# Optimization experiments

Measured on AMD Instinct MI355X. Metric: run time of the kernel, lower is better.

Reference implementation:

```python
import jax, jax.numpy as jnp
import numpy as np

CONF_THRESHOLD = 0.1
CONF_PERCENTILE = 0.5  # 50.0 / 100
VOXEL_SCALES = (10.0, 20.0, 40.0)
ADAPTIVE_LAMBDA = 20.0  # median of voxel_scales
K = 1024                # coords per axis for packing (coords are < ~lambda * extent_ratio << 1024)
SENTINEL = K * K * K    # key for invalid points; > any packed key, fits int32


def setup_inputs() -> dict:
    key = jax.random.key(0)
    k1, k2 = jax.random.split(key)
    world_points = jax.random.normal(k1, (1, 64, 384, 384, 3), dtype=jnp.float32)
    world_points_conf = jax.random.uniform(k2, (1, 64, 384, 384), dtype=jnp.float32)
    return {"world_points": world_points, "world_points_conf": world_points_conf}


def _unique_voxel_counts(pts, valid, pmin, min_extent, voxel_lambda):
    # pts: [S, N, 3], valid: [S, N]
    voxel_size = min_extent / voxel_lambda
    coords = jnp.floor((pts - pmin) / voxel_size).astype(jnp.int32)
    coords = jnp.clip(coords, 0, K - 1)
    packed = (coords[..., 0] * K + coords[..., 1]) * K + coords[..., 2]  # [S, N]
    keys = jnp.where(valid, packed, SENTINEL)
    skeys = jnp.sort(keys, axis=1)
    prev = jnp.concatenate([jnp.full((skeys.shape[0], 1), -1, skeys.dtype), skeys[:, :-1]], axis=1)
    is_new = (skeys != prev) & (skeys < SENTINEL)
    return jnp.sum(is_new, axis=1).astype(jnp.int32)  # [S] unique voxels per frame


def reference(world_points, world_points_conf):
    wp = world_points[0]            # [S, H, W, 3]
    conf = world_points_conf[0]     # [S, H, W]
    S = wp.shape[0]
    pts = wp.reshape(S, -1, 3)      # [S, N, 3]
    c = conf.reshape(S, -1)         # [S, N]

    # per-frame confidence gating: conf > threshold AND conf >= per-frame median
    q = jnp.quantile(c, CONF_PERCENTILE, axis=1, keepdims=True)
    valid = (c > CONF_THRESHOLD) & (c >= q)  # [S, N]

    # global bbox over all valid points (across frames)
    BIG = jnp.float32(1e30)
    vmask = valid[..., None]
    pmin = jnp.min(jnp.where(vmask, pts, BIG), axis=(0, 1))    # [3]
    pmax = jnp.max(jnp.where(vmask, pts, -BIG), axis=(0, 1))   # [3]
    min_extent = jnp.min(pmax - pmin)

    scales = list(VOXEL_SCALES) + [ADAPTIVE_LAMBDA]
    counts = jnp.stack([
        _unique_voxel_counts(pts, valid, pmin, min_extent, lam) for lam in scales
    ], axis=0)  # [n_scales + 1(adaptive), S]

    # scene complexity: std(depths of conf>thr points, unbiased) * density
    mask = (c > CONF_THRESHOLD).astype(pts.dtype)
    depths = jnp.linalg.norm(pts, axis=-1)  # [S, N]
    n = jnp.sum(mask)
    mean_d = jnp.sum(depths * mask) / n
    var_d = jnp.sum(mask * (depths - mean_d) ** 2) / (n - 1.0)  # Bessel, matches torch .std()
    complexity = jnp.sqrt(var_d) * jnp.mean(mask)

    return counts, complexity
```

## Files before the change

kernel.cpp:

```cpp
#include <hip/hip_runtime.h>
#include <cstdint>

#define S_FRAMES 64
#define NPF      147456
#define TOT      (S_FRAMES * NPF)
#define NBINS    4096
#define R1       73728u
#define NB1      512
#define CHK      (NPF / 8)
#define G4       (CHK / 4)
#define CAPC     512
#define CAPR     4096
#define LCAPR    1024
#define LCAPC    128
#define WORDS_BM 9344

#define OFF_HSL  0
#define OFF_CSL  (OFF_HSL + NB1 * NBINS * 4)
#define OFF_PBD  (OFF_CSL + NB1 * 384 * 4)
#define OFF_PBC  (OFF_PBD + NB1 * 16)
#define OFF_CTR  (OFF_PBC + NB1 * 4)
#define OFF_HDR  (OFF_CTR + 128 * 4)
#define OFF_CAND (OFF_HDR + 128 * 4)
#define OFF_RECI (OFF_CAND + S_FRAMES * CAPC * 4)
#define OFF_RECV (OFF_RECI + S_FRAMES * CAPR * 4)
#define OFF_MED  (OFF_RECV + S_FRAMES * CAPR * 4)
#define OFF_FBB  (OFF_MED + 256)
#define OFF_VSL  (((OFF_FBB + S_FRAMES * 6 * 4) + 15) & ~15)

__device__ __forceinline__ int conf_bin(float v) {
    int b = (int)(v * (float)NBINS);
    return b < 0 ? 0 : (b > NBINS - 1 ? NBINS - 1 : b);
}
__device__ __forceinline__ uint32_t encf(float f) {
    uint32_t u = __float_as_uint(f);
    return (u & 0x80000000u) ? ~u : (u | 0x80000000u);
}
__device__ __forceinline__ float decf(uint32_t e) {
    uint32_t u = (e & 0x80000000u) ? (e & 0x7FFFFFFFu) : ~e;
    return __uint_as_float(u);
}

__global__ __launch_bounds__(256) void k_pass1(const float* __restrict__ conf,
                                               const float* __restrict__ pts,
                                               uint32_t* __restrict__ hsl,
                                               uint32_t* __restrict__ csl,
                                               double* __restrict__ pbd,
                                               uint32_t* __restrict__ pbc,
                                               uint32_t* __restrict__ ctr) {
    int f = blockIdx.x >> 3, chunk = blockIdx.x & 7;
    __shared__ uint32_t h[NBINS];
    __shared__ uint32_t cmn[192], cmx[192];
    for (int i = threadIdx.x; i < NBINS; i += 256) h[i] = 0;
    for (int i = threadIdx.x; i < 192; i += 256) { cmn[i] = 0xFFFFFFFFu; cmx[i] = 0u; }
    if (chunk == 0 && threadIdx.x < 2) ctr[f + threadIdx.x * 64] = 0u;
    __syncthreads();

    const size_t base = (size_t)f * NPF + (size_t)chunk * CHK;
    const float4* c4 = (const float4*)(conf + base);
    const float4* p4 = (const float4*)(pts + base * 3);
    double s1 = 0.0, s2 = 0.0;
    uint32_t cnt = 0;
    for (int i = threadIdx.x; i < G4; i += 256) {
        float4 cc = c4[i];
        float4 a = p4[3 * (size_t)i], b = p4[3 * (size_t)i + 1], d = p4[3 * (size_t)i + 2];
        float cv[4] = {cc.x, cc.y, cc.z, cc.w};
        float v[12] = {a.x, a.y, a.z, a.w, b.x, b.y, b.z, b.w, d.x, d.y, d.z, d.w};
        #pragma unroll
        for (int j = 0; j < 4; j++) {
            float c = cv[j];
            int fb = conf_bin(c);
            atomicAdd(&h[fb], 1u);
            if (c > 0.1f) {
                float x = v[3 * j], y = v[3 * j + 1], z = v[3 * j + 2];
                float dd = sqrtf(x * x + y * y + z * z);
                s1 += (double)dd;
                s2 += (double)dd * (double)dd;
                cnt++;
                int cb3 = (fb >> 6) * 3;
                atomicMin(&cmn[cb3 + 0], encf(x));
                atomicMin(&cmn[cb3 + 1], encf(y));
                atomicMin(&cmn[cb3 + 2], encf(z));
                atomicMax(&cmx[cb3 + 0], encf(x));
                atomicMax(&cmx[cb3 + 1], encf(y));
                atomicMax(&cmx[cb3 + 2], encf(z));
            }
        }
    }
    __syncthreads();
    uint32_t* gh = hsl + (size_t)blockIdx.x * NBINS;
    for (int i = threadIdx.x; i < NBINS; i += 256) gh[i] = h[i];
    uint32_t* gc = csl + (size_t)blockIdx.x * 384;
    for (int i = threadIdx.x; i < 192; i += 256) { gc[i] = cmn[i]; gc[192 + i] = cmx[i]; }

    for (int o = 32; o > 0; o >>= 1) {
        s1 += __shfl_xor(s1, o); s2 += __shfl_xor(s2, o); cnt += __shfl_xor(cnt, o);
    }
    __shared__ double rd[2][4];
    __shared__ uint32_t rc[4];
    int wave = threadIdx.x >> 6, lane = threadIdx.x & 63;
    if (lane == 0) { rd[0][wave] = s1; rd[1][wave] = s2; rc[wave] = cnt; }
    __syncthreads();
    if (threadIdx.x == 0) {
        pbd[2 * (size_t)blockIdx.x]     = rd[0][0] + rd[0][1] + rd[0][2] + rd[0][3];
        pbd[2 * (size_t)blockIdx.x + 1] = rd[1][0] + rd[1][1] + rd[1][2] + rd[1][3];
        pbc[blockIdx.x] = rc[0] + rc[1] + rc[2] + rc[3];
    }
}

__global__ __launch_bounds__(1024) void k_resolve(const float* __restrict__ conf,
                                                  const uint32_t* __restrict__ hsl,
                                                  uint32_t* __restrict__ ctr,
                                                  uint32_t* __restrict__ hdr,
                                                  float* __restrict__ cand,
                                                  uint32_t* __restrict__ reci,
                                                  float* __restrict__ recv) {
    int f = blockIdx.x >> 3, chunk = blockIdx.x & 7;
    const int tid = threadIdx.x;
    __shared__ uint32_t h[NBINS];
    __shared__ uint32_t wsum[16], wexcl[16];
    __shared__ uint32_t binfo[2];
    const uint32_t* hb = hsl + (size_t)(f * 8) * NBINS;
    for (int i = tid; i < NBINS; i += 1024) {
        uint32_t s = 0;
        #pragma unroll
        for (int k = 0; k < 8; k++) s += hb[(size_t)k * NBINS + i];
        h[i] = s;
    }
    __syncthreads();
    const int base = tid * 4;
    uint32_t s = h[base] + h[base + 1] + h[base + 2] + h[base + 3];
    const uint32_t lane = tid & 63, wave = tid >> 6;
    uint32_t scan = s;
    for (int o = 1; o < 64; o <<= 1) {
        uint32_t t = __shfl_up(scan, o);
        if (lane >= o) scan += t;
    }
    if (lane == 63) wsum[wave] = scan;
    __syncthreads();
    if (tid == 0) {
        uint32_t run = 0;
        for (int w = 0; w < 16; w++) { wexcl[w] = run; run += wsum[w]; }
    }
    __syncthreads();
    uint32_t excl = wexcl[wave] + (scan - s);
    if (R1 >= excl && R1 < excl + s) {
        uint32_t cum = excl;
        #pragma unroll
        for (int j = 0; j < 4; j++) {
            uint32_t c2 = h[base + j];
            if (R1 < cum + c2) { binfo[0] = (uint32_t)(base + j); binfo[1] = cum; break; }
            cum += c2;
        }
    }
    __syncthreads();
    const int b1 = (int)binfo[0];
    const int bc = b1 >> 6;
    if (chunk == 0 && tid < 2) hdr[f * 2 + tid] = binfo[tid];

    __shared__ uint32_t l_ri[LCAPR];
    __shared__ float    l_rv[LCAPR];
    __shared__ float    l_cv[LCAPC];
    __shared__ uint32_t l_nr, l_nc, g_base_r, g_base_c;
    if (tid == 0) { l_nr = 0u; l_nc = 0u; }
    __syncthreads();

    uint32_t* ccnt = &ctr[f];
    uint32_t* rcnt = &ctr[64 + f];
    const float4* c4 = (const float4*)(conf + (size_t)f * NPF + (size_t)chunk * CHK);
    for (int i = tid; i < G4; i += 1024) {
        float4 v = c4[i];
        float vv[4] = {v.x, v.y, v.z, v.w};
        #pragma unroll
        for (int j = 0; j < 4; j++) {
            int fb = conf_bin(vv[j]);
            if (fb == b1) {
                uint32_t k = atomicAdd(&l_nc, 1u);
                if (k < LCAPC) l_cv[k] = vv[j];
                else {
                    uint32_t g = atomicAdd(ccnt, 1u);
                    if (g < CAPC) cand[(size_t)f * CAPC + g] = vv[j];
                }
            }
            if ((fb >> 6) == bc) {
                uint32_t k = atomicAdd(&l_nr, 1u);
                if (k < LCAPR) {
                    l_ri[k] = (uint32_t)(chunk * CHK + i * 4 + j);
                    l_rv[k] = vv[j];
                } else {
                    uint32_t g = atomicAdd(rcnt, 1u);
                    if (g < CAPR) {
                        reci[(size_t)f * CAPR + g] = (uint32_t)(chunk * CHK + i * 4 + j);
                        recv[(size_t)f * CAPR + g] = vv[j];
                    }
                }
            }
        }
    }
    __syncthreads();
    if (tid == 0) {
        g_base_c = atomicAdd(ccnt, min(l_nc, (uint32_t)LCAPC));
        g_base_r = atomicAdd(rcnt, min(l_nr, (uint32_t)LCAPR));
    }
    __syncthreads();
    uint32_t nc = min(l_nc, (uint32_t)LCAPC), bcg = g_base_c;
    for (uint32_t i = tid; i < nc; i += 1024) {
        uint32_t g = bcg + i;
        if (g < CAPC) cand[(size_t)f * CAPC + g] = l_cv[i];
    }
    uint32_t nr = min(l_nr, (uint32_t)LCAPR), brg = g_base_r;
    for (uint32_t i = tid; i < nr; i += 1024) {
        uint32_t g = brg + i;
        if (g < CAPR) {
            reci[(size_t)f * CAPR + g] = l_ri[i];
            recv[(size_t)f * CAPR + g] = l_rv[i];
        }
    }
}

__global__ __launch_bounds__(1024) void k_frame(const float* __restrict__ pts,
                                                const uint32_t* __restrict__ hdr,
                                                const uint32_t* __restrict__ ctr,
                                                const float* __restrict__ cand,
                                                const uint32_t* __restrict__ reci,
                                                const float* __restrict__ recv,
                                                const uint32_t* __restrict__ csl,
                                                float* __restrict__ med,
                                                float* __restrict__ fbb) {
    int f = blockIdx.x;
    const int tid = threadIdx.x;
    __shared__ float cbuf[CAPC];
    __shared__ float smed;
    int b1 = (int)hdr[f * 2];
    uint32_t cb1 = hdr[f * 2 + 1];
    int bc = b1 >> 6;
    int m = (int)min(ctr[f], (uint32_t)CAPC);
    for (int i = tid; i < m; i += 1024) cbuf[i] = cand[(size_t)f * CAPC + i];
    __syncthreads();
    int target = (int)(R1 - cb1);
    for (int i = tid; i < m; i += 1024) {
        float v = cbuf[i];
        int r = 0;
        for (int j = 0; j < m; j++) {
            float w = cbuf[j];
            r += (w < v) || (w == v && j < i);
        }
        if (r == target) { smed = v; med[f] = v; }
    }
    __syncthreads();
    float mv = smed;

    float mnx = 1e30f, mny = 1e30f, mnz = 1e30f;
    float mxx = -1e30f, mxy = -1e30f, mxz = -1e30f;
    int rn = (int)min(ctr[64 + f], (uint32_t)CAPR);
    for (int k = tid; k < rn; k += 1024) {
        float v = recv[(size_t)f * CAPR + k];
        if (v > 0.1f && v >= mv) {
            size_t idx = ((size_t)f * NPF + reci[(size_t)f * CAPR + k]) * 3;
            float x = pts[idx], y = pts[idx + 1], z = pts[idx + 2];
            mnx = fminf(mnx, x); mny = fminf(mny, y); mnz = fminf(mnz, z);
            mxx = fmaxf(mxx, x); mxy = fmaxf(mxy, y); mxz = fmaxf(mxz, z);
        }
    }
    if (tid < 64 && tid > bc) {
        uint32_t emn[3] = {0xFFFFFFFFu, 0xFFFFFFFFu, 0xFFFFFFFFu};
        uint32_t emx[3] = {0u, 0u, 0u};
        for (int sI = 0; sI < 8; sI++) {
            const uint32_t* gc = csl + (size_t)(f * 8 + sI) * 384;
            #pragma unroll
            for (int k = 0; k < 3; k++) {
                emn[k] = min(emn[k], gc[tid * 3 + k]);
                emx[k] = max(emx[k], gc[192 + tid * 3 + k]);
            }
        }
        if (emn[0] != 0xFFFFFFFFu) {
            mnx = fminf(mnx, decf(emn[0])); mny = fminf(mny, decf(emn[1]));
            mnz = fminf(mnz, decf(emn[2]));
            mxx = fmaxf(mxx, decf(emx[0])); mxy = fmaxf(mxy, decf(emx[1]));
            mxz = fmaxf(mxz, decf(emx[2]));
        }
    }
    for (int o = 32; o > 0; o >>= 1) {
        mnx = fminf(mnx, __shfl_xor(mnx, o)); mny = fminf(mny, __shfl_xor(mny, o));
        mnz = fminf(mnz, __shfl_xor(mnz, o));
        mxx = fmaxf(mxx, __shfl_xor(mxx, o)); mxy = fmaxf(mxy, __shfl_xor(mxy, o));
        mxz = fmaxf(mxz, __shfl_xor(mxz, o));
    }
    __shared__ float rf[6][16];
    int wave = tid >> 6, lane = tid & 63;
    if (lane == 0) {
        rf[0][wave] = mnx; rf[1][wave] = mny; rf[2][wave] = mnz;
        rf[3][wave] = mxx; rf[4][wave] = mxy; rf[5][wave] = mxz;
    }
    __syncthreads();
    if (tid == 0) {
        float o0 = rf[0][0], o1 = rf[1][0], o2 = rf[2][0];
        float o3 = rf[3][0], o4 = rf[4][0], o5 = rf[5][0];
        for (int w = 1; w < 16; w++) {
            o0 = fminf(o0, rf[0][w]); o1 = fminf(o1, rf[1][w]); o2 = fminf(o2, rf[2][w]);
            o3 = fmaxf(o3, rf[3][w]); o4 = fmaxf(o4, rf[4][w]); o5 = fmaxf(o5, rf[5][w]);
        }
        fbb[f * 6 + 0] = o0; fbb[f * 6 + 1] = o1; fbb[f * 6 + 2] = o2;
        fbb[f * 6 + 3] = o3; fbb[f * 6 + 4] = o4; fbb[f * 6 + 5] = o5;
    }
}

__global__ __launch_bounds__(256) void k_voxel(const float* __restrict__ pts,
                                               const float* __restrict__ conf,
                                               const float* __restrict__ med,
                                               const float* __restrict__ fbb,
                                               uint32_t* __restrict__ vsl) {
    int f = blockIdx.x >> 3;
    int chunk = blockIdx.x & 7;
    __shared__ __align__(16) uint32_t bm[WORDS_BM];
    for (int i = threadIdx.x; i < WORDS_BM; i += 256) bm[i] = 0;
    float pmnx = 1e30f, pmny = 1e30f, pmnz = 1e30f;
    float pmxx = -1e30f, pmxy = -1e30f, pmxz = -1e30f;
    for (int i = 0; i < S_FRAMES; i++) {
        pmnx = fminf(pmnx, fbb[i * 6 + 0]); pmny = fminf(pmny, fbb[i * 6 + 1]);
        pmnz = fminf(pmnz, fbb[i * 6 + 2]);
        pmxx = fmaxf(pmxx, fbb[i * 6 + 3]); pmxy = fmaxf(pmxy, fbb[i * 6 + 4]);
        pmxz = fmaxf(pmxz, fbb[i * 6 + 5]);
    }
    float ex = pmxx - pmnx, ey = pmxy - pmny, ez = pmxz - pmnz;
    float me = fminf(ex, fminf(ey, ez));
    float i40 = 40.0f / me, i20 = 20.0f / me, i10 = 10.0f / me;
    float q = med[f];
    __syncthreads();
    const size_t base = (size_t)f * NPF + (size_t)chunk * CHK;
    const float4* c4 = (const float4*)(conf + base);
    const float4* p4 = (const float4*)(pts + base * 3);
    for (int i = threadIdx.x; i < G4; i += 256) {
        float4 cc = c4[i];
        float4 a = p4[3 * (size_t)i], b = p4[3 * (size_t)i + 1], d = p4[3 * (size_t)i + 2];
        float cv[4] = {cc.x, cc.y, cc.z, cc.w};
        float v[12] = {a.x, a.y, a.z, a.w, b.x, b.y, b.z, b.w, d.x, d.y, d.z, d.w};
        #pragma unroll
        for (int j = 0; j < 4; j++) {
            float c = cv[j];
            if (c > 0.1f && c >= q) {
                float x = v[3 * j] - pmnx, y = v[3 * j + 1] - pmny, z = v[3 * j + 2] - pmnz;
                int cx, cy, cz, bit;
                cx = (int)floorf(x * i40); cy = (int)floorf(y * i40); cz = (int)floorf(z * i40);
                cx = min(max(cx, 0), 63); cy = min(max(cy, 0), 63); cz = min(max(cz, 0), 63);
                bit = (cx << 12) | (cy << 6) | cz;
                atomicOr(&bm[bit >> 5], 1u << (bit & 31));
                cx = (int)floorf(x * i20); cy = (int)floorf(y * i20); cz = (int)floorf(z * i20);
                cx = min(max(cx, 0), 31); cy = min(max(cy, 0), 31); cz = min(max(cz, 0), 31);
                bit = (cx << 10) | (cy << 5) | cz;
                atomicOr(&bm[8192 + (bit >> 5)], 1u << (bit & 31));
                cx = (int)floorf(x * i10); cy = (int)floorf(y * i10); cz = (int)floorf(z * i10);
                cx = min(max(cx, 0), 15); cy = min(max(cy, 0), 15); cz = min(max(cz, 0), 15);
                bit = (cx << 8) | (cy << 4) | cz;
                atomicOr(&bm[9216 + (bit >> 5)], 1u << (bit & 31));
            }
        }
    }
    __syncthreads();
    uint4* dst = (uint4*)(vsl + (size_t)blockIdx.x * WORDS_BM);
    const uint4* src = (const uint4*)bm;
    for (int i = threadIdx.x; i < WORDS_BM / 4; i += 256) dst[i] = src[i];
}

__global__ __launch_bounds__(256) void k_final(const uint32_t* __restrict__ vsl,
                                               const double* __restrict__ pbd,
                                               const uint32_t* __restrict__ pbc,
                                               float* __restrict__ out) {
    int f = blockIdx.x;
    uint32_t c40 = 0, c20 = 0, c10 = 0;
    const uint32_t* fb = vsl + (size_t)(f * 8) * WORDS_BM;
    for (int i = threadIdx.x; i < WORDS_BM / 4; i += 256) {
        uint4 w = ((const uint4*)fb)[i];
        #pragma unroll
        for (int k = 1; k < 8; k++) {
            uint4 u = ((const uint4*)(fb + (size_t)k * WORDS_BM))[i];
            w.x |= u.x; w.y |= u.y; w.z |= u.z; w.w |= u.w;
        }
        uint32_t pc = __popc(w.x) + __popc(w.y) + __popc(w.z) + __popc(w.w);
        if (i < 2048) c40 += pc;
        else if (i < 2304) c20 += pc;
        else c10 += pc;
    }
    for (int o = 32; o > 0; o >>= 1) {
        c40 += __shfl_xor(c40, o);
        c20 += __shfl_xor(c20, o);
        c10 += __shfl_xor(c10, o);
    }
    __shared__ uint32_t red[3][4];
    int wave = threadIdx.x >> 6, lane = threadIdx.x & 63;
    if (lane == 0) { red[0][wave] = c40; red[1][wave] = c20; red[2][wave] = c10; }
    __syncthreads();
    if (threadIdx.x == 0) {
        uint32_t t40 = red[0][0] + red[0][1] + red[0][2] + red[0][3];
        uint32_t t20 = red[1][0] + red[1][1] + red[1][2] + red[1][3];
        uint32_t t10 = red[2][0] + red[2][1] + red[2][2] + red[2][3];
        out[0 * S_FRAMES + f] = (float)t10;
        out[1 * S_FRAMES + f] = (float)t20;
        out[2 * S_FRAMES + f] = (float)t40;
        out[3 * S_FRAMES + f] = (float)t20;
    }
    if (f == 0) {
        double s1 = 0.0, s2 = 0.0;
        uint32_t cnt = 0;
        for (int b = threadIdx.x; b < NB1; b += 256) {
            s1 += pbd[2 * (size_t)b];
            s2 += pbd[2 * (size_t)b + 1];
            cnt += pbc[b];
        }
        for (int o = 32; o > 0; o >>= 1) {
            s1 += __shfl_xor(s1, o); s2 += __shfl_xor(s2, o); cnt += __shfl_xor(cnt, o);
        }
        __shared__ double rd[2][4];
        __shared__ uint32_t rc2[4];
        if (lane == 0) { rd[0][wave] = s1; rd[1][wave] = s2; rc2[wave] = cnt; }
        __syncthreads();
        if (threadIdx.x == 0) {
            double S1 = rd[0][0] + rd[0][1] + rd[0][2] + rd[0][3];
            double S2 = rd[1][0] + rd[1][1] + rd[1][2] + rd[1][3];
            double n = (double)(rc2[0] + rc2[1] + rc2[2] + rc2[3]);
            double mean = S1 / n;
            double var = (S2 - n * mean * mean) / (n - 1.0);
            out[4 * S_FRAMES] = (float)(sqrt(var) * (n / (double)TOT));
        }
    }
}

extern "C" void kernel_launch(void* const* d_in, const int* in_sizes, int n_in,
                              void* d_out, int out_size, void* d_ws, size_t ws_size,
                              hipStream_t stream) {
    const float* pts  = (const float*)d_in[0];
    const float* conf = (const float*)d_in[1];
    float* out = (float*)d_out;
    char* ws = (char*)d_ws;
    uint32_t* hsl  = (uint32_t*)(ws + OFF_HSL);
    uint32_t* csl  = (uint32_t*)(ws + OFF_CSL);
    double*   pbd  = (double*)(ws + OFF_PBD);
    uint32_t* pbc  = (uint32_t*)(ws + OFF_PBC);
    uint32_t* ctr  = (uint32_t*)(ws + OFF_CTR);
    uint32_t* hdr  = (uint32_t*)(ws + OFF_HDR);
    float*    cand = (float*)(ws + OFF_CAND);
    uint32_t* reci = (uint32_t*)(ws + OFF_RECI);
    float*    recv = (float*)(ws + OFF_RECV);
    float*    med  = (float*)(ws + OFF_MED);
    float*    fbb  = (float*)(ws + OFF_FBB);
    uint32_t* vsl  = (uint32_t*)(ws + OFF_VSL);

    k_pass1  <<<NB1,      256,  0, stream>>>(conf, pts, hsl, csl, pbd, pbc, ctr);
    k_resolve<<<NB1,      1024, 0, stream>>>(conf, hsl, ctr, hdr, cand, reci, recv);
    k_frame  <<<S_FRAMES, 1024, 0, stream>>>(pts, hdr, ctr, cand, reci, recv, csl, med, fbb);
    k_voxel  <<<NB1,      256,  0, stream>>>(pts, conf, med, fbb, vsl);
    k_final  <<<S_FRAMES, 256,  0, stream>>>(vsl, pbd, pbc, out);
}
```

Baseline: 105.9 us.

## Split histogram bin search into own kernel and retune per-frame slice counts

```diff
diff --git a/kernel.cpp b/kernel.cpp
--- a/kernel.cpp
+++ b/kernel.cpp
@@ -6,9 +6,22 @@
 #define TOT      (S_FRAMES * NPF)
 #define NBINS    4096
 #define R1       73728u
-#define NB1      512
-#define CHK      (NPF / 8)
-#define G4       (CHK / 4)
+
+#define NSL      32
+#define NB1      (S_FRAMES * NSL)
+#define CHK1     (NPF / NSL)
+#define G41      (CHK1 / 4)
+
+#define NRS      8
+#define NBR      (S_FRAMES * NRS)
+#define CHKR     (NPF / NRS)
+#define G4R      (CHKR / 4)
+
+#define NVS      16
+#define NBV      (S_FRAMES * NVS)
+#define CHKV     (NPF / NVS)
+#define G4V      (CHKV / 4)
+
 #define CAPC     512
 #define CAPR     4096
 #define LCAPR    1024
@@ -48,7 +61,7 @@
                                                double* __restrict__ pbd,
                                                uint32_t* __restrict__ pbc,
                                                uint32_t* __restrict__ ctr) {
-    int f = blockIdx.x >> 3, chunk = blockIdx.x & 7;
+    int f = blockIdx.x >> 5, chunk = blockIdx.x & 31;
     __shared__ uint32_t h[NBINS];
     __shared__ uint32_t cmn[192], cmx[192];
     for (int i = threadIdx.x; i < NBINS; i += 256) h[i] = 0;
@@ -56,12 +69,12 @@
     if (chunk == 0 && threadIdx.x < 2) ctr[f + threadIdx.x * 64] = 0u;
     __syncthreads();
 
-    const size_t base = (size_t)f * NPF + (size_t)chunk * CHK;
+    const size_t base = (size_t)f * NPF + (size_t)chunk * CHK1;
     const float4* c4 = (const float4*)(conf + base);
     const float4* p4 = (const float4*)(pts + base * 3);
     double s1 = 0.0, s2 = 0.0;
     uint32_t cnt = 0;
-    for (int i = threadIdx.x; i < G4; i += 256) {
+    for (int i = threadIdx.x; i < G41; i += 256) {
         float4 cc = c4[i];
         float4 a = p4[3 * (size_t)i], b = p4[3 * (size_t)i + 1], d = p4[3 * (size_t)i + 2];
         float cv[4] = {cc.x, cc.y, cc.z, cc.w};
@@ -108,55 +121,56 @@
     }
 }
 
+__global__ __launch_bounds__(1024) void k_findbin(const uint32_t* __restrict__ hsl,
+                                                  uint32_t* __restrict__ hdr) {
+    int f = blockIdx.x;
+    const int tid = threadIdx.x;
+    const uint32_t* hb = hsl + (size_t)(f * NSL) * NBINS;
+    uint4 acc = make_uint4(0u, 0u, 0u, 0u);
+    for (int s = 0; s < NSL; s++) {
+        uint4 u = *(const uint4*)(hb + (size_t)s * NBINS + tid * 4);
+        acc.x += u.x; acc.y += u.y; acc.z += u.z; acc.w += u.w;
+    }
+    uint32_t s4 = acc.x + acc.y + acc.z + acc.w;
+    const uint32_t lane = tid & 63, wave = tid >> 6;
+    uint32_t scan = s4;
+    for (int o = 1; o < 64; o <<= 1) {
+        uint32_t t = __shfl_up(scan, o);
+        if (lane >= o) scan += t;
+    }
+    __shared__ uint32_t wsum[16], wexcl[16];
+    __shared__ uint32_t binfo[2];
+    if (lane == 63) wsum[wave] = scan;
+    __syncthreads();
+    if (tid == 0) {
+        uint32_t run = 0;
+        for (int w = 0; w < 16; w++) { wexcl[w] = run; run += wsum[w]; }
+    }
+    __syncthreads();
+    uint32_t excl = wexcl[wave] + (scan - s4);
+    if (R1 >= excl && R1 < excl + s4) {
+        uint32_t cum = excl;
+        uint32_t bv[4] = {acc.x, acc.y, acc.z, acc.w};
+        #pragma unroll
+        for (int j = 0; j < 4; j++) {
+            if (R1 < cum + bv[j]) { binfo[0] = (uint32_t)(tid * 4 + j); binfo[1] = cum; break; }
+            cum += bv[j];
+        }
+    }
+    __syncthreads();
+    if (tid < 2) hdr[f * 2 + tid] = binfo[tid];
+}
+
 __global__ __launch_bounds__(1024) void k_resolve(const float* __restrict__ conf,
-                                                  const uint32_t* __restrict__ hsl,
+                                                  const uint32_t* __restrict__ hdr,
                                                   uint32_t* __restrict__ ctr,
-                                                  uint32_t* __restrict__ hdr,
                                                   float* __restrict__ cand,
                                                   uint32_t* __restrict__ reci,
                                                   float* __restrict__ recv) {
     int f = blockIdx.x >> 3, chunk = blockIdx.x & 7;
     const int tid = threadIdx.x;
-    __shared__ uint32_t h[NBINS];
-    __shared__ uint32_t wsum[16], wexcl[16];
-    __shared__ uint32_t binfo[2];
-    const uint32_t* hb = hsl + (size_t)(f * 8) * NBINS;
-    for (int i = tid; i < NBINS; i += 1024) {
-        uint32_t s = 0;
-        #pragma unroll
-        for (int k = 0; k < 8; k++) s += hb[(size_t)k * NBINS + i];
-        h[i] = s;
-    }
-    __syncthreads();
-    const int base = tid * 4;
-    uint32_t s = h[base] + h[base + 1] + h[base + 2] + h[base + 3];
-    const uint32_t lane = tid & 63, wave = tid >> 6;
-    uint32_t scan = s;
-    for (int o = 1; o < 64; o <<= 1) {
-        uint32_t t = __shfl_up(scan, o);
-        if (lane >= o) scan += t;
-    }
-    if (lane == 63) wsum[wave] = scan;
-    __syncthreads();
-    if (tid == 0) {
-        uint32_t run = 0;
-        for (int w = 0; w < 16; w++) { wexcl[w] = run; run += wsum[w]; }
-    }
-    __syncthreads();
-    uint32_t excl = wexcl[wave] + (scan - s);
-    if (R1 >= excl && R1 < excl + s) {
-        uint32_t cum = excl;
-        #pragma unroll
-        for (int j = 0; j < 4; j++) {
-            uint32_t c2 = h[base + j];
-            if (R1 < cum + c2) { binfo[0] = (uint32_t)(base + j); binfo[1] = cum; break; }
-            cum += c2;
-        }
-    }
-    __syncthreads();
-    const int b1 = (int)binfo[0];
+    const int b1 = (int)hdr[f * 2];
     const int bc = b1 >> 6;
-    if (chunk == 0 && tid < 2) hdr[f * 2 + tid] = binfo[tid];
 
     __shared__ uint32_t l_ri[LCAPR];
     __shared__ float    l_rv[LCAPR];
@@ -167,8 +181,8 @@
 
     uint32_t* ccnt = &ctr[f];
     uint32_t* rcnt = &ctr[64 + f];
-    const float4* c4 = (const float4*)(conf + (size_t)f * NPF + (size_t)chunk * CHK);
-    for (int i = tid; i < G4; i += 1024) {
+    const float4* c4 = (const float4*)(conf + (size_t)f * NPF + (size_t)chunk * CHKR);
+    for (int i = tid; i < G4R; i += 1024) {
         float4 v = c4[i];
         float vv[4] = {v.x, v.y, v.z, v.w};
         #pragma unroll
@@ -185,12 +199,12 @@
             if ((fb >> 6) == bc) {
                 uint32_t k = atomicAdd(&l_nr, 1u);
                 if (k < LCAPR) {
-                    l_ri[k] = (uint32_t)(chunk * CHK + i * 4 + j);
+                    l_ri[k] = (uint32_t)(chunk * CHKR + i * 4 + j);
                     l_rv[k] = vv[j];
                 } else {
                     uint32_t g = atomicAdd(rcnt, 1u);
                     if (g < CAPR) {
-                        reci[(size_t)f * CAPR + g] = (uint32_t)(chunk * CHK + i * 4 + j);
+                        reci[(size_t)f * CAPR + g] = (uint32_t)(chunk * CHKR + i * 4 + j);
                         recv[(size_t)f * CAPR + g] = vv[j];
                     }
                 }
@@ -265,8 +279,8 @@
     if (tid < 64 && tid > bc) {
         uint32_t emn[3] = {0xFFFFFFFFu, 0xFFFFFFFFu, 0xFFFFFFFFu};
         uint32_t emx[3] = {0u, 0u, 0u};
-        for (int sI = 0; sI < 8; sI++) {
-            const uint32_t* gc = csl + (size_t)(f * 8 + sI) * 384;
+        for (int sI = 0; sI < NSL; sI++) {
+            const uint32_t* gc = csl + (size_t)(f * NSL + sI) * 384;
             #pragma unroll
             for (int k = 0; k < 3; k++) {
                 emn[k] = min(emn[k], gc[tid * 3 + k]);
@@ -310,8 +324,8 @@
                                                const float* __restrict__ med,
                                                const float* __restrict__ fbb,
                                                uint32_t* __restrict__ vsl) {
-    int f = blockIdx.x >> 3;
-    int chunk = blockIdx.x & 7;
+    int f = blockIdx.x >> 4;
+    int chunk = blockIdx.x & 15;
     __shared__ __align__(16) uint32_t bm[WORDS_BM];
     for (int i = threadIdx.x; i < WORDS_BM; i += 256) bm[i] = 0;
     float pmnx = 1e30f, pmny = 1e30f, pmnz = 1e30f;
@@ -327,10 +341,10 @@
     float i40 = 40.0f / me, i20 = 20.0f / me, i10 = 10.0f / me;
     float q = med[f];
     __syncthreads();
-    const size_t base = (size_t)f * NPF + (size_t)chunk * CHK;
+    const size_t base = (size_t)f * NPF + (size_t)chunk * CHKV;
     const float4* c4 = (const float4*)(conf + base);
     const float4* p4 = (const float4*)(pts + base * 3);
-    for (int i = threadIdx.x; i < G4; i += 256) {
+    for (int i = threadIdx.x; i < G4V; i += 256) {
         float4 cc = c4[i];
         float4 a = p4[3 * (size_t)i], b = p4[3 * (size_t)i + 1], d = p4[3 * (size_t)i + 2];
         float cv[4] = {cc.x, cc.y, cc.z, cc.w};
@@ -368,11 +382,10 @@
                                                float* __restrict__ out) {
     int f = blockIdx.x;
     uint32_t c40 = 0, c20 = 0, c10 = 0;
-    const uint32_t* fb = vsl + (size_t)(f * 8) * WORDS_BM;
+    const uint32_t* fb = vsl + (size_t)(f * NVS) * WORDS_BM;
     for (int i = threadIdx.x; i < WORDS_BM / 4; i += 256) {
         uint4 w = ((const uint4*)fb)[i];
-        #pragma unroll
-        for (int k = 1; k < 8; k++) {
+        for (int k = 1; k < NVS; k++) {
             uint4 u = ((const uint4*)(fb + (size_t)k * WORDS_BM))[i];
             w.x |= u.x; w.y |= u.y; w.z |= u.z; w.w |= u.w;
         }
@@ -446,8 +459,9 @@
     uint32_t* vsl  = (uint32_t*)(ws + OFF_VSL);
 
     k_pass1  <<<NB1,      256,  0, stream>>>(conf, pts, hsl, csl, pbd, pbc, ctr);
-    k_resolve<<<NB1,      1024, 0, stream>>>(conf, hsl, ctr, hdr, cand, reci, recv);
+    k_findbin<<<S_FRAMES, 1024, 0, stream>>>(hsl, hdr);
+    k_resolve<<<NBR,      1024, 0, stream>>>(conf, hdr, ctr, cand, reci, recv);
     k_frame  <<<S_FRAMES, 1024, 0, stream>>>(pts, hdr, ctr, cand, reci, recv, csl, med, fbb);
-    k_voxel  <<<NB1,      256,  0, stream>>>(pts, conf, med, fbb, vsl);
+    k_voxel  <<<NBV,      256,  0, stream>>>(pts, conf, med, fbb, vsl);
     k_final  <<<S_FRAMES, 256,  0, stream>>>(vsl, pbd, pbc, out);
 }
```

Result: slower. 113.6 us (+7.4%).
